# Kernel tuning notes

Measured on AMD Instinct MI355X. Metric: run time of the kernel, lower is better.

The kernel has to match this reference:

```python
import jax, jax.numpy as jnp
from jax import lax
import numpy as np

DN = ('NDHWC', 'DHWIO', 'NDHWC')

def _conv(x, W):
    # stride-1 kernel-3 sparse conv on dense grid: SAME conv; absent voxels are zero
    return lax.conv_general_dilated(x, W, (1, 1, 1), 'SAME', dimension_numbers=DN)

def _tconv(x, W):
    # kernel-2 stride-2 generative transpose conv: exactly doubles each spatial dim
    return lax.conv_transpose(x, W, (2, 2, 2), 'VALID', dimension_numbers=DN)

def _pool(h):
    B, D1, D2, D3, C = h.shape
    return h.reshape(B, D1 // 2, 2, D2 // 2, 2, D3 // 2, 2, C).max(axis=(2, 4, 6))

def _pool_mask(m):
    B, D1, D2, D3 = m.shape
    return m.reshape(B, D1 // 2, 2, D2 // 2, 2, D3 // 2, 2).max(axis=(2, 4, 6))

def _up_mask(m):
    return jnp.repeat(jnp.repeat(jnp.repeat(m, 2, axis=1), 2, axis=2), 2, axis=3)

def setup_inputs() -> dict:
    key = jax.random.key(0)
    ks = jax.random.split(key, 6)
    B, G = 2, 128
    x = jax.random.normal(ks[0], (B, G, G, G, 1), dtype=jnp.float32)
    occ = jax.random.randint(ks[1], (B, G, G, G), 0, 10, dtype=jnp.int32)
    def xavier(k, shape):
        fan_in = np.prod(shape[:-1]); fan_out = shape[-1]
        std = np.sqrt(2.0 / (fan_in + fan_out)).astype(np.float32)
        return jax.random.normal(k, shape, dtype=jnp.float32) * std
    W1 = xavier(ks[2], (3, 3, 3, 1, 16))
    W2 = xavier(ks[3], (3, 3, 3, 16, 4))
    Wt1 = xavier(ks[4], (2, 2, 2, 4, 16))
    Wt2 = xavier(ks[5], (2, 2, 2, 16, 1))
    return {"x": x, "W1": W1, "W2": W2, "Wt1": Wt1, "Wt2": Wt2, "occ": occ}

def reference(x, W1, W2, Wt1, Wt2, occ):
    m0 = (occ == 0).astype(x.dtype)            # occupancy mask at full res
    xm = x * m0[..., None]
    h = jax.nn.relu(_conv(xm, W1)) * m0[..., None]   # coords unchanged
    h = _pool(h); m1 = _pool_mask(m0)                # stride-2 max pool on sparse coords
    h = jax.nn.relu(_conv(h, W2)) * m1[..., None]
    h = _pool(h); m2 = _pool_mask(m1)
    m3 = _up_mask(m2)                                # transpose conv emits all children coords
    h = jax.nn.relu(_tconv(h, Wt1)) * m3[..., None]
    m4 = _up_mask(m3)
    out = jax.nn.sigmoid(_tconv(h, Wt2)) * m4[..., None]
    return out
```

## Files before the change

kernel.cpp:

```cpp
#include <hip/hip_runtime.h>
#include <hip/hip_fp16.h>

#define G 128

typedef _Float16 h2_t __attribute__((ext_vector_type(2)));

union U16 { uint4 u; h2_t h2[4]; };
union HV  { uint4 u; h2_t h2[4]; };

__device__ __forceinline__ float dot2f(h2_t a, h2_t b, float c) {
#if __has_builtin(__builtin_amdgcn_fdot2)
    return __builtin_amdgcn_fdot2(a, b, c, false);
#else
    return c + (float)a.x * (float)b.x + (float)a.y * (float)b.y;
#endif
}

__device__ __forceinline__ h2_t h2max(h2_t a, h2_t b) {
#if __has_builtin(__builtin_elementwise_max)
    return __builtin_elementwise_max(a, b);
#else
    h2_t r;
    r.x = a.x > b.x ? a.x : b.x;
    r.y = a.y > b.y ? a.y : b.y;
    return r;
#endif
}

__device__ __forceinline__ float dot4(float4 a, float4 b) {
    return a.x * b.x + a.y * b.y + a.z * b.z + a.w * b.w;
}

__global__ void k_prep(const float* __restrict__ W1, const float* __restrict__ W2,
                       __half* __restrict__ w1h, __half* __restrict__ w2h)
{
    int i = blockIdx.x * 256 + threadIdx.x;
    if (i < 216) {
        int tap = i >> 3, p = i & 7;
        w1h[2 * i]     = __float2half(W1[tap * 16 + 2 * p]);
        w1h[2 * i + 1] = __float2half(W1[tap * 16 + 2 * p + 1]);
    }
    if (i < 864) {
        int t = i >> 5, r = i & 31, co = r >> 3, p = r & 7;
        w2h[2 * i]     = __float2half(W2[t * 64 + (2 * p) * 4 + co]);
        w2h[2 * i + 1] = __float2half(W2[t * 64 + (2 * p + 1) * 4 + co]);
    }
}

__global__ __launch_bounds__(256, 4)
void k_conv1_pool(const float* __restrict__ x, const int* __restrict__ occ,
                  const h2_t* __restrict__ w1h,
                  __half* __restrict__ h1p, float* __restrict__ m1)
{
    __shared__ __align__(16) _Float16      sx[10 * 18 * 24];
    __shared__ __align__(4)  unsigned char smB[10 * 18 * 24];
    __shared__ __align__(16) int           pacc[16 * 256];
    __shared__ unsigned short              slist[2048];
    __shared__ int                         scnt;

    const int bx = blockIdx.x, by = blockIdx.y;
    const int b  = blockIdx.z >> 4, zt = blockIdx.z & 15;
    const int tid = threadIdx.x;

    const int z0 = zt * 8 - 1, y0 = by * 16 - 1;
    const int base_b = b * G * G * G;

    if (tid == 0) scnt = 0;

    {
        uint4 z4 = make_uint4(0u, 0u, 0u, 0u);
        uint4* p4 = (uint4*)pacc;
        p4[tid] = z4; p4[tid + 256] = z4; p4[tid + 512] = z4; p4[tid + 768] = z4;
    }

    #pragma unroll
    for (int it = 0; it < 5; ++it) {
        int c = it * 256 + tid;
        if (c < 1080) {
            int row = c / 6, seg = c - row * 6;
            int lz  = row / 18, ly = row - lz * 18;
            int gz = z0 + lz, gy = y0 + ly;
            int gxc = (bx << 4) - 4 + (seg << 2);
            int4   o4 = make_int4(1, 1, 1, 1);
            float4 x4 = make_float4(0.f, 0.f, 0.f, 0.f);
            if ((unsigned)gz < 128u && (unsigned)gy < 128u && (unsigned)gxc < 128u) {
                const int gi = base_b + (gz * G + gy) * G + gxc;
                o4 = *(const int4*)(occ + gi);
                x4 = *(const float4*)(x + gi);
            }
            unsigned mbits = (o4.x == 0 ? 0x1u : 0u) | (o4.y == 0 ? 0x100u : 0u)
                           | (o4.z == 0 ? 0x10000u : 0u) | (o4.w == 0 ? 0x1000000u : 0u);
            h2_t p01, p23;
            p01.x = (o4.x == 0) ? (_Float16)x4.x : (_Float16)0.f;
            p01.y = (o4.y == 0) ? (_Float16)x4.y : (_Float16)0.f;
            p23.x = (o4.z == 0) ? (_Float16)x4.z : (_Float16)0.f;
            p23.y = (o4.w == 0) ? (_Float16)x4.w : (_Float16)0.f;
            const int eo = row * 24 + (seg << 2);
            union { uint2 u; h2_t h[2]; } pk;
            pk.h[0] = p01; pk.h[1] = p23;
            *(uint2*)&sx[eo] = pk.u;
            *(unsigned*)&smB[eo] = mbits;
        }
    }
    __syncthreads();

    const int tx = tid & 7, ty = (tid >> 3) & 7, tz = tid >> 6;
    const int lane = tid & 63;
    int anym = 0;

    #pragma unroll
    for (int pos = 0; pos < 8; ++pos) {
        const int dz = pos >> 2, dy = (pos >> 1) & 1, dx = pos & 1;
        const int cz = 2 * tz + dz, cy = 2 * ty + dy, cx = 2 * tx + dx;
        const int act = smB[((cz + 1) * 18 + (cy + 1)) * 24 + cx + 4];
        anym |= act;
        unsigned long long bal = __ballot(act != 0);
        int wtot = __popcll(bal);
        int wbase = 0;
        if (lane == 0 && wtot) wbase = atomicAdd(&scnt, wtot);
        wbase = __shfl(wbase, 0);
        if (act) {
            int pre = __popcll(bal & ((1ull << lane) - 1ull));
            slist[wbase + pre] = (unsigned short)((cz << 8) | (cy << 4) | cx);
        }
    }
    __syncthreads();

    const int n = scnt;

    const h2_t zero = (h2_t)(_Float16)0.f;
    for (int kb = 0; kb < n; kb += 256) {
        const int idx = kb + tid;
        if (idx < n) {
            const int code = slist[idx];
            const int cz = code >> 8, cy = (code >> 4) & 15, cx = code & 15;
            const int sb = ((cz + 1) * 18 + (cy + 1)) * 24 + cx + 4;
            h2_t acc[8];
            #pragma unroll
            for (int c = 0; c < 8; ++c) acc[c] = zero;
            #pragma unroll
            for (int kz = 0; kz < 3; ++kz)
            #pragma unroll
            for (int ky = 0; ky < 3; ++ky)
            #pragma unroll
            for (int kx = 0; kx < 3; ++kx) {
                _Float16 v = sx[sb + (kz - 1) * 432 + (ky - 1) * 24 + (kx - 1)];
                h2_t v2 = {v, v};
                const h2_t* w = &w1h[((kz * 3 + ky) * 3 + kx) * 8];
                #pragma unroll
                for (int c = 0; c < 8; ++c) acc[c] = v2 * w[c] + acc[c];
            }
            const int cell = (cz >> 1) * 64 + (cy >> 1) * 8 + (cx >> 1);
            #pragma unroll
            for (int c = 0; c < 8; ++c) {
                float fa = fmaxf((float)acc[c].x, 0.f);
                float fb = fmaxf((float)acc[c].y, 0.f);
                atomicMax(&pacc[(2 * c) * 256 + cell],     __float_as_int(fa));
                atomicMax(&pacc[(2 * c + 1) * 256 + cell], __float_as_int(fb));
            }
        }
    }
    __syncthreads();

    const int pz = zt * 4 + tz, py = by * 8 + ty, px = bx * 8 + tx;
    const int vidx = ((b * 64 + pz) * 64 + py) * 64 + px;
    HV p0, p1;
    #pragma unroll
    for (int c = 0; c < 4; ++c) {
        h2_t a, bq;
        a.x  = (_Float16)__int_as_float(pacc[(2 * c) * 256 + tid]);
        a.y  = (_Float16)__int_as_float(pacc[(2 * c + 1) * 256 + tid]);
        bq.x = (_Float16)__int_as_float(pacc[(8 + 2 * c) * 256 + tid]);
        bq.y = (_Float16)__int_as_float(pacc[(9 + 2 * c) * 256 + tid]);
        p0.h2[c] = a; p1.h2[c] = bq;
    }
    uint4* o = (uint4*)&h1p[(size_t)vidx * 16];
    o[0] = p0.u;
    o[1] = p1.u;
    m1[vidx] = anym ? 1.f : 0.f;
}

__global__ __launch_bounds__(256)
void k_conv2_dec(const __half* __restrict__ h1p, const float* __restrict__ m1,
                 const h2_t* __restrict__ w2h,
                 const float* __restrict__ Wt1, const float* __restrict__ Wt2,
                 float* __restrict__ out)
{
    __shared__ uint4  tile[1100];
    __shared__ float4 wt1[128];
    __shared__ float4 wt2[32];
    __shared__ float4 sh_h[64];
    __shared__ float  sh_m[64];

    const int bx = blockIdx.x, by = blockIdx.y;
    const int b  = blockIdx.z >> 3, bz = blockIdx.z & 7;
    const int tid = threadIdx.x;

    if (tid < 128) wt1[tid] = ((const float4*)Wt1)[tid];
    if (tid < 32)  wt2[tid] = ((const float4*)Wt2)[tid];

    const int z0 = bz * 8 - 1, y0 = by * 8 - 1, x0 = bx * 8 - 1;

    const int dy = tid & 1, dz = (tid >> 1) & 1;
    const int qx = (tid >> 2) & 3, Y = (tid >> 4) & 3, Z = (tid >> 6) & 3;
    const int cx0 = 2 * qx, cy = 2 * Y + dy, cz = 2 * Z + dz;

    float acc[2][4] = {{0.f, 0.f, 0.f, 0.f}, {0.f, 0.f, 0.f, 0.f}};

    for (int h = 0; h < 2; ++h) {
        if (h) __syncthreads();
        #pragma unroll
        for (int it = 0; it < 5; ++it) {
            int g = it * 256 + tid;
            if (g < 1100) {
                int z = g / 110, r = g - z * 110, y = r / 11, xx = r - y * 11;
                int gz = z0 + z, gy = y0 + y, gx = x0 + xx;
                uint4 a = make_uint4(0u, 0u, 0u, 0u);
                if ((unsigned)gz < 64u && (unsigned)gy < 64u && (unsigned)gx < 64u)
                    a = ((const uint4*)&h1p[(size_t)(((b * 64 + gz) * 64 + gy) * 64 + gx) * 16])[h];
                tile[g] = a;
            }
        }
        __syncthreads();

        #pragma unroll
        for (int kz = 0; kz < 3; ++kz)
        #pragma unroll
        for (int ky = 0; ky < 3; ++ky) {
            const int rb = (cz + kz) * 110 + (cy + ky) * 11 + cx0;
            h2_t hp[4][4];
            #pragma unroll
            for (int xi = 0; xi < 4; ++xi) {
                U16 a; a.u = tile[rb + xi];
                #pragma unroll
                for (int p = 0; p < 4; ++p) hp[xi][p] = a.h2[p];
            }
            const int t3 = (kz * 3 + ky) * 3;
            #pragma unroll
            for (int kx = 0; kx < 3; ++kx) {
                const h2_t* w = w2h + (t3 + kx) * 32 + 4 * h;
                #pragma unroll
                for (int j = 0; j < 2; ++j) {
                    #pragma unroll
                    for (int co = 0; co < 4; ++co) {
                        float a = acc[j][co];
                        #pragma unroll
                        for (int p = 0; p < 4; ++p)
                            a = dot2f(hp[kx + j][p], w[co * 8 + p], a);
                        acc[j][co] = a;
                    }
                }
            }
        }
    }

    const int gcz = bz * 8 + cz, gcy = by * 8 + cy, gcx = bx * 8 + cx0;
    const float mv0 = m1[((b * 64 + gcz) * 64 + gcy) * 64 + gcx];
    const float mv1 = m1[((b * 64 + gcz) * 64 + gcy) * 64 + gcx + 1];
    float m = fmaxf(mv0, mv1);
    float r0 = fmaxf(fmaxf(acc[0][0], 0.f) * mv0, fmaxf(acc[1][0], 0.f) * mv1);
    float r1 = fmaxf(fmaxf(acc[0][1], 0.f) * mv0, fmaxf(acc[1][1], 0.f) * mv1);
    float r2 = fmaxf(fmaxf(acc[0][2], 0.f) * mv0, fmaxf(acc[1][2], 0.f) * mv1);
    float r3 = fmaxf(fmaxf(acc[0][3], 0.f) * mv0, fmaxf(acc[1][3], 0.f) * mv1);

    #pragma unroll
    for (int mask = 1; mask <= 2; mask <<= 1) {
        r0 = fmaxf(r0, __shfl_xor(r0, mask));
        r1 = fmaxf(r1, __shfl_xor(r1, mask));
        r2 = fmaxf(r2, __shfl_xor(r2, mask));
        r3 = fmaxf(r3, __shfl_xor(r3, mask));
        m  = fmaxf(m,  __shfl_xor(m,  mask));
    }
    if ((tid & 3) == 0) {
        int p = Z * 16 + Y * 4 + qx;
        sh_h[p] = make_float4(r0, r1, r2, r3);
        sh_m[p] = m;
    }
    __syncthreads();

    {
        const int p  = tid >> 2;
        const int a  = (tid >> 1) & 1;
        const int bb = tid & 1;
        const int pZ = p >> 4, pY = (p >> 2) & 3, pq = p & 3;
        const int pz = bz * 4 + pZ, py = by * 4 + pY, pxq = bx * 4 + pq;

        const float mm = sh_m[p];
        const float4 hv = sh_h[p];

        const int b0q = ((((1 - a) * 2 + (1 - bb)) * 2) + 1) * 16;
        const int b1q = ((((1 - a) * 2 + (1 - bb)) * 2) + 0) * 16;
        float4 t0q[4], t1q[4];
        #pragma unroll
        for (int q = 0; q < 4; ++q) {
            float4 a0 = wt1[b0q + q],      a1 = wt1[b0q + 4 + q];
            float4 a2 = wt1[b0q + 8 + q],  a3 = wt1[b0q + 12 + q];
            float4 c0 = wt1[b1q + q],      c1 = wt1[b1q + 4 + q];
            float4 c2 = wt1[b1q + 8 + q],  c3 = wt1[b1q + 12 + q];
            float4 s0, s1;
            s0.x = hv.x * a0.x + hv.y * a1.x + hv.z * a2.x + hv.w * a3.x;
            s0.y = hv.x * a0.y + hv.y * a1.y + hv.z * a2.y + hv.w * a3.y;
            s0.z = hv.x * a0.z + hv.y * a1.z + hv.z * a2.z + hv.w * a3.z;
            s0.w = hv.x * a0.w + hv.y * a1.w + hv.z * a2.w + hv.w * a3.w;
            s1.x = hv.x * c0.x + hv.y * c1.x + hv.z * c2.x + hv.w * c3.x;
            s1.y = hv.x * c0.y + hv.y * c1.y + hv.z * c2.y + hv.w * c3.y;
            s1.z = hv.x * c0.z + hv.y * c1.z + hv.z * c2.z + hv.w * c3.z;
            s1.w = hv.x * c0.w + hv.y * c1.w + hv.z * c2.w + hv.w * c3.w;
            t0q[q] = make_float4(fmaxf(s0.x, 0.f), fmaxf(s0.y, 0.f),
                                 fmaxf(s0.z, 0.f), fmaxf(s0.w, 0.f));
            t1q[q] = make_float4(fmaxf(s1.x, 0.f), fmaxf(s1.y, 0.f),
                                 fmaxf(s1.z, 0.f), fmaxf(s1.w, 0.f));
        }

        #pragma unroll
        for (int e = 0; e < 2; ++e) {
            #pragma unroll
            for (int f = 0; f < 2; ++f) {
                const int d  = 4 * pz + 2 * a + e;
                const int hh = 4 * py + 2 * bb + f;
                const int be = ((1 - e) * 2 + (1 - f)) * 2;
                const float4* wg0 = &wt2[(be + 1) * 4];
                const float4* wg1 = &wt2[(be + 0) * 4];
                float s00 = dot4(t0q[0], wg0[0]) + dot4(t0q[1], wg0[1])
                          + dot4(t0q[2], wg0[2]) + dot4(t0q[3], wg0[3]);
                float s01 = dot4(t0q[0], wg1[0]) + dot4(t0q[1], wg1[1])
                          + dot4(t0q[2], wg1[2]) + dot4(t0q[3], wg1[3]);
                float s10 = dot4(t1q[0], wg0[0]) + dot4(t1q[1], wg0[1])
                          + dot4(t1q[2], wg0[2]) + dot4(t1q[3], wg0[3]);
                float s11 = dot4(t1q[0], wg1[0]) + dot4(t1q[1], wg1[1])
                          + dot4(t1q[2], wg1[2]) + dot4(t1q[3], wg1[3]);
                float4 o;
                o.x = mm / (1.f + __expf(-s00));
                o.y = mm / (1.f + __expf(-s01));
                o.z = mm / (1.f + __expf(-s10));
                o.w = mm / (1.f + __expf(-s11));
                *(float4*)&out[((b * G + d) * G + hh) * G + 4 * pxq] = o;
            }
        }
    }
}

extern "C" void kernel_launch(void* const* d_in, const int* in_sizes, int n_in,
                              void* d_out, int out_size, void* d_ws, size_t ws_size,
                              hipStream_t stream) {
    (void)in_sizes; (void)n_in; (void)out_size; (void)ws_size;
    const float* x   = (const float*)d_in[0];
    const float* W1  = (const float*)d_in[1];
    const float* W2  = (const float*)d_in[2];
    const float* Wt1 = (const float*)d_in[3];
    const float* Wt2 = (const float*)d_in[4];
    const int*   occ = (const int*)d_in[5];
    float* out = (float*)d_out;

    char* ws = (char*)d_ws;
    __half* h1p = (__half*)ws;
    float*  m1  = (float*)(ws + 8388608ull * sizeof(__half));
    __half* w2h = (__half*)(m1 + 524288);
    __half* w1h = w2h + 1728;

    k_prep<<<dim3(4), dim3(256), 0, stream>>>(W1, W2, w1h, w2h);
    k_conv1_pool<<<dim3(8, 8, 32), dim3(256), 0, stream>>>(x, occ, (const h2_t*)w1h, h1p, m1);
    k_conv2_dec<<<dim3(8, 8, 16), dim3(256), 0, stream>>>(h1p, m1, (const h2_t*)w2h, Wt1, Wt2, out);
}
```

Measured before the change: 144.0 us.

## Drop weight-prep kernel, prefetch tiles into registers, single-pass conv2

Removes the separate k_prep launch: each block now converts W1 and W2 to fp16 into shared memory itself. Both kernels issue their global tile loads into registers up front, before the shared-memory init and weight staging, so load latency overlaps that setup. Conv1 builds its active list directly during staging with per-thread shared atomics, dropping the mask buffer and the ballot pass. Conv2 loads both channel halves into a doubled shared tile and makes one pass, removing a barrier and reload. The cost is more registers and shared memory per block, which may lower occupancy.

After: 205.8 us. +42.9%, slower.

```diff
diff --git a/kernel.cpp b/kernel.cpp
--- a/kernel.cpp
+++ b/kernel.cpp
@@ -7,6 +7,7 @@
 
 union U16 { uint4 u; h2_t h2[4]; };
 union HV  { uint4 u; h2_t h2[4]; };
+union PK2 { uint2 u; h2_t h[2]; };
 
 __device__ __forceinline__ float dot2f(h2_t a, h2_t b, float c) {
 #if __has_builtin(__builtin_amdgcn_fdot2)
@@ -16,46 +17,20 @@
 #endif
 }
 
-__device__ __forceinline__ h2_t h2max(h2_t a, h2_t b) {
-#if __has_builtin(__builtin_elementwise_max)
-    return __builtin_elementwise_max(a, b);
-#else
-    h2_t r;
-    r.x = a.x > b.x ? a.x : b.x;
-    r.y = a.y > b.y ? a.y : b.y;
-    return r;
-#endif
-}
-
 __device__ __forceinline__ float dot4(float4 a, float4 b) {
     return a.x * b.x + a.y * b.y + a.z * b.z + a.w * b.w;
 }
 
-__global__ void k_prep(const float* __restrict__ W1, const float* __restrict__ W2,
-                       __half* __restrict__ w1h, __half* __restrict__ w2h)
-{
-    int i = blockIdx.x * 256 + threadIdx.x;
-    if (i < 216) {
-        int tap = i >> 3, p = i & 7;
-        w1h[2 * i]     = __float2half(W1[tap * 16 + 2 * p]);
-        w1h[2 * i + 1] = __float2half(W1[tap * 16 + 2 * p + 1]);
-    }
-    if (i < 864) {
-        int t = i >> 5, r = i & 31, co = r >> 3, p = r & 7;
-        w2h[2 * i]     = __float2half(W2[t * 64 + (2 * p) * 4 + co]);
-        w2h[2 * i + 1] = __float2half(W2[t * 64 + (2 * p + 1) * 4 + co]);
-    }
-}
-
 __global__ __launch_bounds__(256, 4)
 void k_conv1_pool(const float* __restrict__ x, const int* __restrict__ occ,
-                  const h2_t* __restrict__ w1h,
+                  const float* __restrict__ W1,
                   __half* __restrict__ h1p, float* __restrict__ m1)
 {
     __shared__ __align__(16) _Float16      sx[10 * 18 * 24];
-    __shared__ __align__(4)  unsigned char smB[10 * 18 * 24];
     __shared__ __align__(16) int           pacc[16 * 256];
-    __shared__ unsigned short              slist[2048];
+    __shared__ __align__(4)  unsigned short slist[2048];
+    __shared__ __align__(16) h2_t          w1L[216];
+    __shared__ __align__(4)  unsigned char sm1[256];
     __shared__ int                         scnt;
 
     const int bx = blockIdx.x, by = blockIdx.y;
@@ -65,13 +40,35 @@
     const int z0 = zt * 8 - 1, y0 = by * 16 - 1;
     const int base_b = b * G * G * G;
 
+    int4   ro[5];
+    float4 rx[5];
+    #pragma unroll
+    for (int it = 0; it < 5; ++it) {
+        int c = it * 256 + tid;
+        int cc = c < 1080 ? c : 1079;
+        int row = cc / 6, seg = cc - row * 6;
+        int lz  = row / 18, ly = row - lz * 18;
+        int gz = z0 + lz, gy = y0 + ly;
+        int gxc = (bx << 4) - 4 + (seg << 2);
+        bool inb = (unsigned)gz < 128u && (unsigned)gy < 128u && (unsigned)gxc < 128u;
+        int gi = inb ? base_b + (gz * G + gy) * G + gxc : base_b;
+        ro[it] = *(const int4*)(occ + gi);
+        rx[it] = *(const float4*)(x + gi);
+    }
+
     if (tid == 0) scnt = 0;
-
     {
         uint4 z4 = make_uint4(0u, 0u, 0u, 0u);
         uint4* p4 = (uint4*)pacc;
         p4[tid] = z4; p4[tid + 256] = z4; p4[tid + 512] = z4; p4[tid + 768] = z4;
     }
+    if (tid < 64) ((unsigned*)sm1)[tid] = 0u;
+    if (tid < 216) {
+        float2 f = ((const float2*)W1)[tid];
+        h2_t w; w.x = (_Float16)f.x; w.y = (_Float16)f.y;
+        w1L[tid] = w;
+    }
+    __syncthreads();
 
     #pragma unroll
     for (int it = 0; it < 5; ++it) {
@@ -81,47 +78,36 @@
             int lz  = row / 18, ly = row - lz * 18;
             int gz = z0 + lz, gy = y0 + ly;
             int gxc = (bx << 4) - 4 + (seg << 2);
-            int4   o4 = make_int4(1, 1, 1, 1);
-            float4 x4 = make_float4(0.f, 0.f, 0.f, 0.f);
-            if ((unsigned)gz < 128u && (unsigned)gy < 128u && (unsigned)gxc < 128u) {
-                const int gi = base_b + (gz * G + gy) * G + gxc;
-                o4 = *(const int4*)(occ + gi);
-                x4 = *(const float4*)(x + gi);
-            }
-            unsigned mbits = (o4.x == 0 ? 0x1u : 0u) | (o4.y == 0 ? 0x100u : 0u)
-                           | (o4.z == 0 ? 0x10000u : 0u) | (o4.w == 0 ? 0x1000000u : 0u);
+            bool inb = (unsigned)gz < 128u && (unsigned)gy < 128u && (unsigned)gxc < 128u;
+            int4   o4 = ro[it];
+            float4 x4 = rx[it];
+            if (!inb) o4 = make_int4(1, 1, 1, 1);
             h2_t p01, p23;
             p01.x = (o4.x == 0) ? (_Float16)x4.x : (_Float16)0.f;
             p01.y = (o4.y == 0) ? (_Float16)x4.y : (_Float16)0.f;
             p23.x = (o4.z == 0) ? (_Float16)x4.z : (_Float16)0.f;
             p23.y = (o4.w == 0) ? (_Float16)x4.w : (_Float16)0.f;
-            const int eo = row * 24 + (seg << 2);
-            union { uint2 u; h2_t h[2]; } pk;
-            pk.h[0] = p01; pk.h[1] = p23;
-            *(uint2*)&sx[eo] = pk.u;
-            *(unsigned*)&smB[eo] = mbits;
-        }
-    }
-    __syncthreads();
-
-    const int tx = tid & 7, ty = (tid >> 3) & 7, tz = tid >> 6;
-    const int lane = tid & 63;
-    int anym = 0;
-
-    #pragma unroll
-    for (int pos = 0; pos < 8; ++pos) {
-        const int dz = pos >> 2, dy = (pos >> 1) & 1, dx = pos & 1;
-        const int cz = 2 * tz + dz, cy = 2 * ty + dy, cx = 2 * tx + dx;
-        const int act = smB[((cz + 1) * 18 + (cy + 1)) * 24 + cx + 4];
-        anym |= act;
-        unsigned long long bal = __ballot(act != 0);
-        int wtot = __popcll(bal);
-        int wbase = 0;
-        if (lane == 0 && wtot) wbase = atomicAdd(&scnt, wtot);
-        wbase = __shfl(wbase, 0);
-        if (act) {
-            int pre = __popcll(bal & ((1ull << lane) - 1ull));
-            slist[wbase + pre] = (unsigned short)((cz << 8) | (cy << 4) | cx);
+            PK2 pk; pk.h[0] = p01; pk.h[1] = p23;
+            *(uint2*)&sx[row * 24 + (seg << 2)] = pk.u;
+
+            if ((unsigned)(lz - 1) < 8u && (unsigned)(ly - 1) < 16u &&
+                (unsigned)(seg - 1) < 4u) {
+                int mb = (o4.x == 0 ? 1 : 0) | (o4.y == 0 ? 2 : 0) |
+                         (o4.z == 0 ? 4 : 0) | (o4.w == 0 ? 8 : 0);
+                if (mb) {
+                    int cnt  = __popc(mb);
+                    int base = atomicAdd(&scnt, cnt);
+                    int cz = lz - 1, cy = ly - 1, cx0v = (seg << 2) - 4;
+                    int cellb = (cz >> 1) * 64 + (cy >> 1) * 8;
+                    #pragma unroll
+                    for (int j = 0; j < 4; ++j) {
+                        if (mb & (1 << j)) {
+                            slist[base++] = (unsigned short)((cz << 8) | (cy << 4) | (cx0v + j));
+                            sm1[cellb + ((cx0v + j) >> 1)] = (unsigned char)1;
+                        }
+                    }
+                }
+            }
         }
     }
     __syncthreads();
@@ -146,22 +132,23 @@
             for (int kx = 0; kx < 3; ++kx) {
                 _Float16 v = sx[sb + (kz - 1) * 432 + (ky - 1) * 24 + (kx - 1)];
                 h2_t v2 = {v, v};
-                const h2_t* w = &w1h[((kz * 3 + ky) * 3 + kx) * 8];
+                const h2_t* w = &w1L[((kz * 3 + ky) * 3 + kx) * 8];
                 #pragma unroll
                 for (int c = 0; c < 8; ++c) acc[c] = v2 * w[c] + acc[c];
             }
             const int cell = (cz >> 1) * 64 + (cy >> 1) * 8 + (cx >> 1);
             #pragma unroll
             for (int c = 0; c < 8; ++c) {
-                float fa = fmaxf((float)acc[c].x, 0.f);
-                float fb = fmaxf((float)acc[c].y, 0.f);
-                atomicMax(&pacc[(2 * c) * 256 + cell],     __float_as_int(fa));
-                atomicMax(&pacc[(2 * c + 1) * 256 + cell], __float_as_int(fb));
-            }
-        }
-    }
-    __syncthreads();
-
+                atomicMax(&pacc[(2 * c) * 256 + cell],
+                          __float_as_int(fmaxf((float)acc[c].x, 0.f)));
+                atomicMax(&pacc[(2 * c + 1) * 256 + cell],
+                          __float_as_int(fmaxf((float)acc[c].y, 0.f)));
+            }
+        }
+    }
+    __syncthreads();
+
+    const int tx = tid & 7, ty = (tid >> 3) & 7, tz = tid >> 6;
     const int pz = zt * 4 + tz, py = by * 8 + ty, px = bx * 8 + tx;
     const int vidx = ((b * 64 + pz) * 64 + py) * 64 + px;
     HV p0, p1;
@@ -177,18 +164,19 @@
     uint4* o = (uint4*)&h1p[(size_t)vidx * 16];
     o[0] = p0.u;
     o[1] = p1.u;
-    m1[vidx] = anym ? 1.f : 0.f;
+    m1[vidx] = sm1[tid] ? 1.f : 0.f;
 }
 
 __global__ __launch_bounds__(256)
 void k_conv2_dec(const __half* __restrict__ h1p, const float* __restrict__ m1,
-                 const h2_t* __restrict__ w2h,
+                 const float* __restrict__ W2,
                  const float* __restrict__ Wt1, const float* __restrict__ Wt2,
                  float* __restrict__ out)
 {
-    __shared__ uint4  tile[1100];
+    __shared__ uint4  tile[2200];
     __shared__ float4 wt1[128];
     __shared__ float4 wt2[32];
+    __shared__ __align__(16) h2_t w2L[864];
     __shared__ float4 sh_h[64];
     __shared__ float  sh_m[64];
 
@@ -196,10 +184,50 @@
     const int b  = blockIdx.z >> 3, bz = blockIdx.z & 7;
     const int tid = threadIdx.x;
 
+    const int z0 = bz * 8 - 1, y0 = by * 8 - 1, x0 = bx * 8 - 1;
+
+    uint4 ra[5], rb4[5];
+    #pragma unroll
+    for (int it = 0; it < 5; ++it) {
+        int g = it * 256 + tid;
+        int gg = g < 1100 ? g : 1099;
+        int z = gg / 110, r = gg - z * 110, y = r / 11, xx = r - y * 11;
+        int gz = z0 + z, gy = y0 + y, gx = x0 + xx;
+        bool inb = (unsigned)gz < 64u && (unsigned)gy < 64u && (unsigned)gx < 64u;
+        size_t vi = inb ? (size_t)(((b * 64 + gz) * 64 + gy) * 64 + gx) : 0;
+        const uint4* src = (const uint4*)&h1p[vi * 16];
+        ra[it]  = src[0];
+        rb4[it] = src[1];
+    }
+
     if (tid < 128) wt1[tid] = ((const float4*)Wt1)[tid];
     if (tid < 32)  wt2[tid] = ((const float4*)Wt2)[tid];
-
-    const int z0 = bz * 8 - 1, y0 = by * 8 - 1, x0 = bx * 8 - 1;
+    #pragma unroll
+    for (int it = 0; it < 4; ++it) {
+        int i = it * 256 + tid;
+        if (i < 864) {
+            int t = i >> 5, rr = i & 31, co = rr >> 3, p = rr & 7;
+            h2_t w;
+            w.x = (_Float16)W2[t * 64 + (2 * p) * 4 + co];
+            w.y = (_Float16)W2[t * 64 + (2 * p + 1) * 4 + co];
+            w2L[i] = w;
+        }
+    }
+
+    #pragma unroll
+    for (int it = 0; it < 5; ++it) {
+        int g = it * 256 + tid;
+        if (g < 1100) {
+            int z = g / 110, r = g - z * 110, y = r / 11, xx = r - y * 11;
+            int gz = z0 + z, gy = y0 + y, gx = x0 + xx;
+            bool inb = (unsigned)gz < 64u && (unsigned)gy < 64u && (unsigned)gx < 64u;
+            uint4 a0 = ra[it], a1 = rb4[it];
+            if (!inb) { a0 = make_uint4(0u, 0u, 0u, 0u); a1 = a0; }
+            tile[g]        = a0;
+            tile[1100 + g] = a1;
+        }
+    }
+    __syncthreads();
 
     const int dy = tid & 1, dz = (tid >> 1) & 1;
     const int qx = (tid >> 2) & 3, Y = (tid >> 4) & 3, Z = (tid >> 6) & 3;
@@ -207,48 +235,35 @@
 
     float acc[2][4] = {{0.f, 0.f, 0.f, 0.f}, {0.f, 0.f, 0.f, 0.f}};
 
-    for (int h = 0; h < 2; ++h) {
-        if (h) __syncthreads();
-        #pragma unroll
-        for (int it = 0; it < 5; ++it) {
-            int g = it * 256 + tid;
-            if (g < 1100) {
-                int z = g / 110, r = g - z * 110, y = r / 11, xx = r - y * 11;
-                int gz = z0 + z, gy = y0 + y, gx = x0 + xx;
-                uint4 a = make_uint4(0u, 0u, 0u, 0u);
-                if ((unsigned)gz < 64u && (unsigned)gy < 64u && (unsigned)gx < 64u)
-                    a = ((const uint4*)&h1p[(size_t)(((b * 64 + gz) * 64 + gy) * 64 + gx) * 16])[h];
-                tile[g] = a;
-            }
-        }
-        __syncthreads();
-
-        #pragma unroll
-        for (int kz = 0; kz < 3; ++kz)
-        #pragma unroll
-        for (int ky = 0; ky < 3; ++ky) {
-            const int rb = (cz + kz) * 110 + (cy + ky) * 11 + cx0;
-            h2_t hp[4][4];
-            #pragma unroll
-            for (int xi = 0; xi < 4; ++xi) {
-                U16 a; a.u = tile[rb + xi];
+    #pragma unroll
+    for (int kz = 0; kz < 3; ++kz)
+    #pragma unroll
+    for (int ky = 0; ky < 3; ++ky) {
+        const int rb = (cz + kz) * 110 + (cy + ky) * 11 + cx0;
+        h2_t hp[2][4][4];
+        #pragma unroll
+        for (int hh = 0; hh < 2; ++hh)
+        #pragma unroll
+        for (int xi = 0; xi < 4; ++xi) {
+            U16 a; a.u = tile[hh * 1100 + rb + xi];
+            #pragma unroll
+            for (int p = 0; p < 4; ++p) hp[hh][xi][p] = a.h2[p];
+        }
+        const int t3 = (kz * 3 + ky) * 3;
+        #pragma unroll
+        for (int kx = 0; kx < 3; ++kx) {
+            const h2_t* w = &w2L[(t3 + kx) * 32];
+            #pragma unroll
+            for (int j = 0; j < 2; ++j) {
                 #pragma unroll
-                for (int p = 0; p < 4; ++p) hp[xi][p] = a.h2[p];
-            }
-            const int t3 = (kz * 3 + ky) * 3;
-            #pragma unroll
-            for (int kx = 0; kx < 3; ++kx) {
-                const h2_t* w = w2h + (t3 + kx) * 32 + 4 * h;
-                #pragma unroll
-                for (int j = 0; j < 2; ++j) {
+                for (int co = 0; co < 4; ++co) {
+                    float a = acc[j][co];
                     #pragma unroll
-                    for (int co = 0; co < 4; ++co) {
-                        float a = acc[j][co];
-                        #pragma unroll
-                        for (int p = 0; p < 4; ++p)
-                            a = dot2f(hp[kx + j][p], w[co * 8 + p], a);
-                        acc[j][co] = a;
-                    }
+                    for (int hh = 0; hh < 2; ++hh)
+                    #pragma unroll
+                    for (int p = 0; p < 4; ++p)
+                        a = dot2f(hp[hh][kx + j][p], w[co * 8 + 4 * hh + p], a);
+                    acc[j][co] = a;
                 }
             }
         }
@@ -355,10 +370,7 @@
     char* ws = (char*)d_ws;
     __half* h1p = (__half*)ws;
     float*  m1  = (float*)(ws + 8388608ull * sizeof(__half));
-    __half* w2h = (__half*)(m1 + 524288);
-    __half* w1h = w2h + 1728;
-
-    k_prep<<<dim3(4), dim3(256), 0, stream>>>(W1, W2, w1h, w2h);
-    k_conv1_pool<<<dim3(8, 8, 32), dim3(256), 0, stream>>>(x, occ, (const h2_t*)w1h, h1p, m1);
-    k_conv2_dec<<<dim3(8, 8, 16), dim3(256), 0, stream>>>(h1p, m1, (const h2_t*)w2h, Wt1, Wt2, out);
-}
+
+    k_conv1_pool<<<dim3(8, 8, 32), dim3(256), 0, stream>>>(x, occ, W1, h1p, m1);
+    k_conv2_dec<<<dim3(8, 8, 16), dim3(256), 0, stream>>>(h1p, m1, W2, Wt1, Wt2, out);
+}
```
